# Optimization experiments

Hardware: AMD Instinct MI355X
Metric: run time of the kernel (lower is better)

Reference implementation:

```python
import jax, jax.numpy as jnp
import numpy as np

B, S, DIM = 2, 2048, 2048
H, DH = 16, 128            # head_dim = dim // n_heads; decop_rot_dim == head_dim (required by the view)
LKV, LQ = 512, 1024        # latent kv / q compression dims


def setup_inputs() -> dict:
    key = jax.random.key(0)
    ks = jax.random.split(key, 12)
    w = lambda k, shape: jax.random.normal(k, shape, jnp.float32) * 0.02
    x = jax.random.normal(ks[0], (B, S, DIM), jnp.float32)
    # rotary table: angles[t, i] = t * 10000^(-2i/DH), complex passed as cos/sin pair
    inv_freq = 1.0 / (10000.0 ** (np.arange(0, DH, 2, dtype=np.float64) / DH))
    ang = np.outer(np.arange(S, dtype=np.float64), inv_freq)  # [S, DH/2]
    return {
        "x": x,
        "freq_cos": jnp.asarray(np.cos(ang), jnp.float32),
        "freq_sin": jnp.asarray(np.sin(ang), jnp.float32),
        "w_lq": w(ks[1], (LQ, DIM)),
        "w_lkv": w(ks[2], (LKV, DIM)),
        "w_q": w(ks[3], (H * DH, LQ)),
        "w_k": w(ks[4], (H * DH, LKV)),
        "w_v": w(ks[5], (H * DH, LKV)),
        "w_qr": w(ks[6], (H * DH, LQ)),
        "b_qr": w(ks[7], (H * DH,)),
        "w_kr": w(ks[8], (H * DH, DIM)),
        "b_kr": w(ks[9], (H * DH,)),
        "w_o": w(ks[10], (DIM, H * DH)),
        "b_o": w(ks[11], (DIM,)),
    }


def _rope(t, freq):
    # t: [B,S,H,DH]; freq: [S,DH/2] complex. Pairs (even,odd) along last dim rotated.
    b, s, h, d = t.shape
    tc = t.astype(jnp.float32).reshape(b, s, h, d // 2, 2)
    tc = jax.lax.complex(tc[..., 0], tc[..., 1]) * freq[None, :, None, :]
    return jnp.stack([jnp.real(tc), jnp.imag(tc)], axis=-1).reshape(b, s, h, d).astype(t.dtype)


def reference(x, freq_cos, freq_sin, w_lq, w_lkv, w_q, w_k, w_v, w_qr, b_qr, w_kr, b_kr, w_o, b_o):
    b, s, _ = x.shape
    freq = jax.lax.complex(freq_cos, freq_sin)          # [S, DH/2]
    cq = x @ w_lq.T                                      # [B,S,LQ]
    ckv = x @ w_lkv.T                                    # [B,S,LKV]
    q = (cq @ w_q.T).reshape(b, s, H, DH)
    qr = _rope((cq @ w_qr.T + b_qr).reshape(b, s, H, DH), freq)
    k = (ckv @ w_k.T).reshape(b, s, H, DH)
    kr = _rope((x @ w_kr.T + b_kr).reshape(b, s, H, DH), freq)
    v = (ckv @ w_v.T).reshape(b, s, H, DH)
    q = jnp.concatenate([q, qr], axis=-1)                # [B,S,H,2*DH]
    k = jnp.concatenate([k, kr], axis=-1)
    # note: scale uses sqrt(head_dim), NOT sqrt(2*head_dim), faithful to source
    scores = jnp.einsum('bqhd,bkhd->bhqk', q, k) / jnp.sqrt(jnp.float32(DH))
    att = jax.nn.softmax(scores.astype(jnp.float32), axis=-1).astype(q.dtype)
    out = jnp.einsum('bhqk,bkhd->bqhd', att, v).reshape(b, s, H * DH)
    return out @ w_o.T + b_o
```

## Files before the change

kernel.cpp:

```cpp
#include <hip/hip_runtime.h>
#include <hip/hip_bf16.h>


#define Bb 2
#define Ss 2048
#define DIMd 2048
#define Hh 16
#define DHd 128

typedef __hip_bfloat16 bf16;
typedef __attribute__((ext_vector_type(8))) short short8;
typedef __attribute__((ext_vector_type(4))) float floatx4;

#define MFMA(a, b, c) __builtin_amdgcn_mfma_f32_16x16x32_bf16((a), (b), (c), 0, 0, 0)

__device__ __forceinline__ void async16(const bf16* g, bf16* l) {
  __builtin_amdgcn_global_load_lds(
      (const __attribute__((address_space(1))) unsigned int*)g,
      (__attribute__((address_space(3))) unsigned int*)l, 16, 0, 0);
}

__global__ __launch_bounds__(256) void cvt_all(
    const float* x, const float* wlq, const float* wlkv, const float* wq,
    const float* wqr, const float* wk, const float* wv, const float* wkr,
    const float* wo, bf16* dx, bf16* dwlq, bf16* dwlkv, bf16* dwq, bf16* dwqr,
    bf16* dwk, bf16* dwv, bf16* dwkr, bf16* dwo) {
  long i = (long)blockIdx.x * 256 + threadIdx.x;
  const float* src;
  bf16* dst;
  long base;
  if (i < 2097152L)      { src = x;    dst = dx;    base = 0; }
  else if (i < 2621440L) { src = wlq;  dst = dwlq;  base = 2097152L; }
  else if (i < 2883584L) { src = wlkv; dst = dwlkv; base = 2621440L; }
  else if (i < 3407872L) { src = wq;   dst = dwq;   base = 2883584L; }
  else if (i < 3932160L) { src = wqr;  dst = dwqr;  base = 3407872L; }
  else if (i < 4194304L) { src = wk;   dst = dwk;   base = 3932160L; }
  else if (i < 4456448L) { src = wv;   dst = dwv;   base = 4194304L; }
  else if (i < 5505024L) { src = wkr;  dst = dwkr;  base = 4456448L; }
  else                   { src = wo;   dst = dwo;   base = 5505024L; }
  long j = i - base;
  float4 f = ((const float4*)src)[j];
  union { ushort4 u4; bf16 h[4]; } cv;
  cv.h[0] = __float2bfloat16(f.x);
  cv.h[1] = __float2bfloat16(f.y);
  cv.h[2] = __float2bfloat16(f.z);
  cv.h[3] = __float2bfloat16(f.w);
  ((ushort4*)dst)[j] = cv.u4;
}

template <int MODE>
__device__ __forceinline__ void gemm_body(const bf16* __restrict__ A,
                                          const bf16* __restrict__ Bw,
                                          const float* __restrict__ bias,
                                          void* __restrict__ Cout,
                                          void* __restrict__ Cout2,
                                          const float* __restrict__ fco,
                                          const float* __restrict__ fsi,
                                          int M, int N, int K, int lda) {
  extern __shared__ __align__(16) bf16 smem[];
  bf16* As = smem;
  bf16* Bs = smem + 8192;
  const int tid = threadIdx.x;
  const int lane = tid & 63;
  const int w = tid >> 6;
  const int wm = w & 1, wn = w >> 1;
  const int m0 = blockIdx.y * 128, n0 = blockIdx.x * 128;
  const int lr = lane & 15, lg = lane >> 4;

  floatx4 acc[4][4];
#pragma unroll
  for (int mi = 0; mi < 4; ++mi)
#pragma unroll
    for (int ni = 0; ni < 4; ++ni)
#pragma unroll
      for (int r = 0; r < 4; ++r) acc[mi][ni][r] = 0.f;

  for (int k0 = 0; k0 < K; k0 += 64) {
    __syncthreads();
#pragma unroll
    for (int i = 0; i < 4; ++i) {
      int c = i * 256 + tid;
      int row = c >> 3;
      int cg = (c & 7) ^ (row & 7);
      async16(A + (size_t)(m0 + row) * lda + k0 + cg * 8, As + (i * 256 + w * 64) * 8);
      async16(Bw + (size_t)(n0 + row) * K + k0 + cg * 8, Bs + (i * 256 + w * 64) * 8);
    }
    __syncthreads();

#pragma unroll
    for (int ks = 0; ks < 2; ++ks) {
      short8 af[4], bfr[4];
#pragma unroll
      for (int mi = 0; mi < 4; ++mi) {
        int row = wm * 64 + mi * 16 + lr;
        af[mi] = *(const short8*)&As[row * 64 + (((ks * 4 + lg) ^ (lr & 7)) * 8)];
      }
#pragma unroll
      for (int ni = 0; ni < 4; ++ni) {
        int row = wn * 64 + ni * 16 + lr;
        bfr[ni] = *(const short8*)&Bs[row * 64 + (((ks * 4 + lg) ^ (lr & 7)) * 8)];
      }
#pragma unroll
      for (int mi = 0; mi < 4; ++mi)
#pragma unroll
        for (int ni = 0; ni < 4; ++ni)
          acc[mi][ni] = MFMA(af[mi], bfr[ni], acc[mi][ni]);
    }
  }

  if (MODE == 5 && n0 >= 2048) {
    __syncthreads();
#pragma unroll
    for (int mi = 0; mi < 4; ++mi)
#pragma unroll
      for (int ni = 0; ni < 4; ++ni)
#pragma unroll
        for (int r = 0; r < 4; ++r) {
          int ml = wm * 64 + mi * 16 + lg * 4 + r;
          int nl = wn * 64 + ni * 16 + lr;
          smem[ml * 129 + nl] = __float2bfloat16(acc[mi][ni][r]);
        }
    __syncthreads();
    int bb = m0 >> 11, s0 = m0 & 2047;
    int hh = (n0 - 2048) >> 7;
    short* vbase = (short*)Cout2 + ((size_t)(bb * Hh + hh) * 128) * Ss;
#pragma unroll
    for (int pa = 0; pa < 8; ++pa) {
      int d = pa * 16 + (tid >> 4);
      int sc = (tid & 15) * 8;
      short8 v;
#pragma unroll
      for (int i = 0; i < 8; ++i) v[i] = *(const short*)&smem[(sc + i) * 129 + d];
      *(short8*)(vbase + (size_t)d * Ss + s0 + sc) = v;
    }
    return;
  }

#pragma unroll
  for (int mi = 0; mi < 4; ++mi)
#pragma unroll
    for (int ni = 0; ni < 4; ++ni)
#pragma unroll
      for (int r = 0; r < 4; ++r) {
        int m = m0 + wm * 64 + mi * 16 + lg * 4 + r;
        int n = n0 + wn * 64 + ni * 16 + lr;
        float v = acc[mi][ni][r];
        int bb = m >> 11, s = m & 2047;
        if (MODE == 3) {
          v += bias[n];
          ((float*)Cout)[(size_t)m * N + n] = v;
        } else if (MODE == 4) {
          if (n < 2048) {
            int hh = n >> 7, d = n & 127;
            ((bf16*)Cout)[((size_t)((bb * Hh + hh) * Ss + s)) * 256 + d] =
                __float2bfloat16(v);
          } else {
            int n2 = n - 2048;
            int hh = n2 >> 7, d = n2 & 127;
            v += bias[n2];
            float vp = __shfl_xor(v, 1, 64);
            float co = fco[s * 64 + (d >> 1)];
            float sn = fsi[s * 64 + (d >> 1)];
            v = (d & 1) ? (v * co + vp * sn) : (v * co - vp * sn);
            ((bf16*)Cout)[((size_t)((bb * Hh + hh) * Ss + s)) * 256 + 128 + d] =
                __float2bfloat16(v);
          }
        } else if (MODE == 5) {
          int hh = n >> 7, d = n & 127;
          ((bf16*)Cout)[((size_t)((bb * Hh + hh) * Ss + s)) * 256 + d] =
              __float2bfloat16(v);
        } else if (MODE == 6) {
          if (n < 1536) {
            ((bf16*)Cout)[(size_t)m * 1536 + n] = __float2bfloat16(v);
          } else {
            int n2 = n - 1536;
            int hh = n2 >> 7, d = n2 & 127;
            v += bias[n2];
            float vp = __shfl_xor(v, 1, 64);
            float co = fco[s * 64 + (d >> 1)];
            float sn = fsi[s * 64 + (d >> 1)];
            v = (d & 1) ? (v * co + vp * sn) : (v * co - vp * sn);
            ((bf16*)Cout2)[((size_t)((bb * Hh + hh) * Ss + s)) * 256 + 128 + d] =
                __float2bfloat16(v);
          }
        }
      }
}

template <int MODE>
__global__ __launch_bounds__(256, 4) void gemm_bt(const bf16* __restrict__ A,
                                                  const bf16* __restrict__ Bw,
                                                  const float* __restrict__ bias,
                                                  void* __restrict__ Cout,
                                                  void* __restrict__ Cout2,
                                                  const float* __restrict__ fco,
                                                  const float* __restrict__ fsi,
                                                  int M, int N, int K, int lda) {
  gemm_body<MODE>(A, Bw, bias, Cout, Cout2, fco, fsi, M, N, K, lda);
}

__global__ __launch_bounds__(256, 4) void gemm_qkv(const bf16* __restrict__ ccat,
                                                   const bf16* __restrict__ wqcat,
                                                   const bf16* __restrict__ wkvcat,
                                                   const float* __restrict__ bqr,
                                                   void* __restrict__ qcat,
                                                   void* __restrict__ kcat,
                                                   void* __restrict__ vt,
                                                   const float* __restrict__ fco,
                                                   const float* __restrict__ fsi) {
  if (blockIdx.z == 0)
    gemm_body<4>(ccat, wqcat, bqr, qcat, nullptr, fco, fsi, 4096, 4096, 1024, 1536);
  else
    gemm_body<5>(ccat + 1024, wkvcat, nullptr, kcat, vt, nullptr, nullptr, 4096, 4096, 512, 1536);
}

__global__ __launch_bounds__(256) void flash_attn(const bf16* __restrict__ Q,
                                                  const bf16* __restrict__ Kc,
                                                  const bf16* __restrict__ Vt,
                                                  bf16* __restrict__ Oa) {
  const float SCALE = 0.08838834764831845f;
  __shared__ __align__(16) bf16 Ks[64 * 256];
  __shared__ __align__(16) bf16 Vs[128 * 64];
  __shared__ __align__(16) bf16 pbuf[4][16 * 64];

  const int lane = threadIdx.x & 63;
  const int w = threadIdx.x >> 6;
  const int lr = lane & 15, lg = lane >> 4;
  const int m7 = lr & 7;
  const int bh = blockIdx.x;
  const int b = bh >> 4, h = bh & 15;
  const int q0 = blockIdx.y * 64 + w * 16;

  const bf16* Qb = Q + (size_t)bh * Ss * 256;
  const bf16* Kb = Kc + (size_t)bh * Ss * 256;
  const bf16* Vb = Vt + (size_t)bh * 128 * Ss;

  short8 qf[8];
  {
    const short* Qrow = (const short*)Qb + (size_t)(q0 + lr) * 256;
#pragma unroll
    for (int kk = 0; kk < 8; ++kk) qf[kk] = *(const short8*)(Qrow + kk * 32 + lg * 8);
  }

  float l_r[4];
  floatx4 oacc[8];
#pragma unroll
  for (int r = 0; r < 4; ++r) l_r[r] = 0.f;
#pragma unroll
  for (int nb = 0; nb < 8; ++nb)
#pragma unroll
    for (int r = 0; r < 4; ++r) oacc[nb][r] = 0.f;

  for (int j0 = 0; j0 < Ss; j0 += 64) {
    __syncthreads();
#pragma unroll
    for (int i = 0; i < 8; ++i) {
      int r = w * 16 + i * 2 + (lane >> 5);
      int cg = (lane & 31) ^ (r & 7);
      async16(Kb + (size_t)(j0 + r) * 256 + cg * 8, Ks + (w * 16 + i * 2) * 256);
    }
#pragma unroll
    for (int i = 0; i < 4; ++i) {
      int r = w * 32 + i * 8 + (lane >> 3);
      int cg = (lane & 7) ^ (r & 7);
      async16(Vb + (size_t)r * Ss + j0 + cg * 8, Vs + (w * 32 + i * 8) * 64);
    }
    __syncthreads();

    floatx4 sf[4];
#pragma unroll
    for (int cb = 0; cb < 4; ++cb)
#pragma unroll
      for (int r = 0; r < 4; ++r) sf[cb][r] = 0.f;
#pragma unroll
    for (int cb = 0; cb < 4; ++cb) {
      const short* Krow = (const short*)Ks + (cb * 16 + lr) * 256;
#pragma unroll
      for (int kk = 0; kk < 8; ++kk) {
        short8 kf = *(const short8*)(Krow + ((4 * kk + lg) ^ m7) * 8);
        sf[cb] = MFMA(qf[kk], kf, sf[cb]);
      }
    }

#pragma unroll
    for (int r = 0; r < 4; ++r) {
      float p0 = __expf(sf[0][r] * SCALE);
      float p1 = __expf(sf[1][r] * SCALE);
      float p2 = __expf(sf[2][r] * SCALE);
      float p3 = __expf(sf[3][r] * SCALE);
      sf[0][r] = p0; sf[1][r] = p1; sf[2][r] = p2; sf[3][r] = p3;
      l_r[r] += (p0 + p1) + (p2 + p3);
    }

    bf16* pb = pbuf[w];
#pragma unroll
    for (int cb = 0; cb < 4; ++cb)
#pragma unroll
      for (int r = 0; r < 4; ++r) {
        int row = lg * 4 + r;
        int ch = (2 * cb + (lr >> 3)) ^ (row & 7);
        pb[row * 64 + ch * 8 + m7] = __float2bfloat16(sf[cb][r]);
      }
    short8 pa[2];
#pragma unroll
    for (int kb = 0; kb < 2; ++kb)
      pa[kb] = *(const short8*)((const short*)pb + lr * 64 + ((4 * kb + lg) ^ m7) * 8);

#pragma unroll
    for (int nb = 0; nb < 8; ++nb) {
#pragma unroll
      for (int kb = 0; kb < 2; ++kb) {
        short8 vf = *(const short8*)((const short*)Vs + (nb * 16 + lr) * 64 +
                                     ((4 * kb + lg) ^ m7) * 8);
        oacc[nb] = MFMA(pa[kb], vf, oacc[nb]);
      }
    }
  }

  float inv_l[4];
#pragma unroll
  for (int r = 0; r < 4; ++r) {
    float s = l_r[r];
    s += __shfl_xor(s, 1, 64);
    s += __shfl_xor(s, 2, 64);
    s += __shfl_xor(s, 4, 64);
    s += __shfl_xor(s, 8, 64);
    inv_l[r] = 1.f / s;
  }
#pragma unroll
  for (int nb = 0; nb < 8; ++nb)
#pragma unroll
    for (int r = 0; r < 4; ++r) {
      int s = q0 + lg * 4 + r;
      int d = nb * 16 + lr;
      Oa[((size_t)(b * Ss + s)) * (Hh * 128) + h * 128 + d] =
          __float2bfloat16(oacc[nb][r] * inv_l[r]);
    }
}

extern "C" void kernel_launch(void* const* d_in, const int* in_sizes, int n_in,
                              void* d_out, int out_size, void* d_ws, size_t ws_size,
                              hipStream_t stream) {
  const float* x    = (const float*)d_in[0];
  const float* fco  = (const float*)d_in[1];
  const float* fsi  = (const float*)d_in[2];
  const float* wlq  = (const float*)d_in[3];
  const float* wlkv = (const float*)d_in[4];
  const float* wq   = (const float*)d_in[5];
  const float* wk   = (const float*)d_in[6];
  const float* wv   = (const float*)d_in[7];
  const float* wqr  = (const float*)d_in[8];
  const float* bqr  = (const float*)d_in[9];
  const float* wkr  = (const float*)d_in[10];
  const float* bkr  = (const float*)d_in[11];
  const float* wo   = (const float*)d_in[12];
  const float* bo   = (const float*)d_in[13];

  char* ws = (char*)d_ws;
  size_t o = 0;
  bf16* x_b    = (bf16*)(ws + o); o += (size_t)Bb * Ss * DIMd * 2;
  bf16* wbig   = (bf16*)(ws + o); o += (size_t)3584 * 2048 * 2;
  bf16* wqcat  = (bf16*)(ws + o); o += (size_t)4096 * 1024 * 2;
  bf16* wkvcat = (bf16*)(ws + o); o += (size_t)4096 * 512 * 2;
  bf16* wo_b   = (bf16*)(ws + o); o += (size_t)2048 * 2048 * 2;
  bf16* ccat   = (bf16*)(ws + o); o += (size_t)4096 * 1536 * 2;
  bf16* qcat   = (bf16*)(ws + o); o += (size_t)Bb * Hh * Ss * 256 * 2;
  bf16* kcat   = (bf16*)(ws + o); o += (size_t)Bb * Hh * Ss * 256 * 2;
  bf16* vt     = (bf16*)(ws + o); o += (size_t)Bb * Hh * 128 * Ss * 2;
  bf16* attn   = (bf16*)(ws + o); o += (size_t)4096 * 2048 * 2;

  cvt_all<<<25600, 256, 0, stream>>>(
      x, wlq, wlkv, wq, wqr, wk, wv, wkr, wo,
      x_b,
      wbig,
      wbig + (size_t)1024 * 2048,
      wqcat,
      wqcat + (size_t)2048 * 1024,
      wkvcat,
      wkvcat + (size_t)2048 * 512,
      wbig + (size_t)1536 * 2048,
      wo_b);

  const int M = Bb * Ss;
  const int GEMM_LDS = 128 * 129 * 2;
  gemm_bt<6><<<dim3(28, 32), 256, GEMM_LDS, stream>>>(
      x_b, wbig, bkr, ccat, kcat, fco, fsi, M, 3584, 2048, 2048);
  gemm_qkv<<<dim3(32, 32, 2), 256, GEMM_LDS, stream>>>(
      ccat, wqcat, wkvcat, bqr, qcat, kcat, vt, fco, fsi);

  flash_attn<<<dim3(Bb * Hh, Ss / 64), 256, 0, stream>>>(qcat, kcat, vt, attn);

  gemm_bt<3><<<dim3(16, 32), 256, GEMM_LDS, stream>>>(
      attn, wo_b, bo, (float*)d_out, nullptr, nullptr, nullptr, M, 2048, 2048, 2048);
}
```

Baseline: 510.8 us.

## Rework flash attention around 32x32 MFMA with register-resident P via lane shuffles

The attention kernel now uses 32x32x16 bf16 MFMA with each wave handling 32 query rows, so a block covers 128 rows and the grid halves. S is computed transposed (K as the A operand), which lets P be packed to bf16 in registers and exchanged across half-waves with shuffles instead of a round trip through an LDS buffer. It also switches to exp2 with a folded scale and precomputes swizzled LDS pointers. The intent is to double K/V reuse per LDS load, cut instruction count and drop the P staging through LDS. In exchange it uses more registers (launch bounds set to 2 blocks) and launches fewer blocks, which lowers occupancy.

```diff
diff --git a/kernel.cpp b/kernel.cpp
--- a/kernel.cpp
+++ b/kernel.cpp
@@ -11,8 +11,10 @@
 typedef __hip_bfloat16 bf16;
 typedef __attribute__((ext_vector_type(8))) short short8;
 typedef __attribute__((ext_vector_type(4))) float floatx4;
+typedef __attribute__((ext_vector_type(16))) float floatx16;
 
 #define MFMA(a, b, c) __builtin_amdgcn_mfma_f32_16x16x32_bf16((a), (b), (c), 0, 0, 0)
+#define MFMA32(a, b, c) __builtin_amdgcn_mfma_f32_32x32x16_bf16((a), (b), (c), 0, 0, 0)
 
 __device__ __forceinline__ void async16(const bf16* g, bf16* l) {
   __builtin_amdgcn_global_load_lds(
@@ -214,42 +216,53 @@
     gemm_body<5>(ccat + 1024, wkvcat, nullptr, kcat, vt, nullptr, nullptr, 4096, 4096, 512, 1536);
 }
 
-__global__ __launch_bounds__(256) void flash_attn(const bf16* __restrict__ Q,
-                                                  const bf16* __restrict__ Kc,
-                                                  const bf16* __restrict__ Vt,
-                                                  bf16* __restrict__ Oa) {
-  const float SCALE = 0.08838834764831845f;
+__global__ __launch_bounds__(256, 2) void flash_attn(const bf16* __restrict__ Q,
+                                                     const bf16* __restrict__ Kc,
+                                                     const bf16* __restrict__ Vt,
+                                                     bf16* __restrict__ Oa) {
+  const float CE = 0.08838834764831845f * 1.4426950408889634f;
   __shared__ __align__(16) bf16 Ks[64 * 256];
   __shared__ __align__(16) bf16 Vs[128 * 64];
-  __shared__ __align__(16) bf16 pbuf[4][16 * 64];
 
   const int lane = threadIdx.x & 63;
   const int w = threadIdx.x >> 6;
-  const int lr = lane & 15, lg = lane >> 4;
-  const int m7 = lr & 7;
+  const int m = lane & 31;
+  const int hi = lane >> 5;
   const int bh = blockIdx.x;
   const int b = bh >> 4, h = bh & 15;
-  const int q0 = blockIdx.y * 64 + w * 16;
+  const int q0 = blockIdx.y * 128 + w * 32;
 
   const bf16* Qb = Q + (size_t)bh * Ss * 256;
   const bf16* Kb = Kc + (size_t)bh * Ss * 256;
   const bf16* Vb = Vt + (size_t)bh * 128 * Ss;
 
-  short8 qf[8];
+  short8 qf[16];
   {
-    const short* Qrow = (const short*)Qb + (size_t)(q0 + lr) * 256;
-#pragma unroll
-    for (int kk = 0; kk < 8; ++kk) qf[kk] = *(const short8*)(Qrow + kk * 32 + lg * 8);
+    const short* Qrow = (const short*)Qb + (size_t)(q0 + m) * 256 + hi * 8;
+#pragma unroll
+    for (int dt = 0; dt < 16; ++dt) qf[dt] = *(const short8*)(Qrow + dt * 16);
   }
 
-  float l_r[4];
-  floatx4 oacc[8];
-#pragma unroll
-  for (int r = 0; r < 4; ++r) l_r[r] = 0.f;
-#pragma unroll
-  for (int nb = 0; nb < 8; ++nb)
-#pragma unroll
-    for (int r = 0; r < 4; ++r) oacc[nb][r] = 0.f;
+  const int key = m & 7;
+  const short* kp[2][4];
+#pragma unroll
+  for (int cbt = 0; cbt < 2; ++cbt)
+#pragma unroll
+    for (int dl = 0; dl < 4; ++dl)
+      kp[cbt][dl] = (const short*)Ks + (cbt * 32 + m) * 256 + (((2 * dl + hi) ^ key) * 8);
+  const short* vp[4];
+#pragma unroll
+  for (int kb = 0; kb < 4; ++kb)
+    vp[kb] = (const short*)Vs + m * 64 + (((2 * kb + hi) ^ key) * 8);
+
+  float l = 0.f;
+  floatx16 oacc[4];
+#pragma unroll
+  for (int nb = 0; nb < 4; ++nb)
+#pragma unroll
+    for (int r = 0; r < 16; ++r) oacc[nb][r] = 0.f;
+
+  const bool lo = (lane < 32);
 
   for (int j0 = 0; j0 < Ss; j0 += 64) {
     __syncthreads();
@@ -267,75 +280,68 @@
     }
     __syncthreads();
 
-    floatx4 sf[4];
-#pragma unroll
-    for (int cb = 0; cb < 4; ++cb)
-#pragma unroll
-      for (int r = 0; r < 4; ++r) sf[cb][r] = 0.f;
-#pragma unroll
-    for (int cb = 0; cb < 4; ++cb) {
-      const short* Krow = (const short*)Ks + (cb * 16 + lr) * 256;
-#pragma unroll
-      for (int kk = 0; kk < 8; ++kk) {
-        short8 kf = *(const short8*)(Krow + ((4 * kk + lg) ^ m7) * 8);
-        sf[cb] = MFMA(qf[kk], kf, sf[cb]);
-      }
-    }
-
-#pragma unroll
-    for (int r = 0; r < 4; ++r) {
-      float p0 = __expf(sf[0][r] * SCALE);
-      float p1 = __expf(sf[1][r] * SCALE);
-      float p2 = __expf(sf[2][r] * SCALE);
-      float p3 = __expf(sf[3][r] * SCALE);
-      sf[0][r] = p0; sf[1][r] = p1; sf[2][r] = p2; sf[3][r] = p3;
-      l_r[r] += (p0 + p1) + (p2 + p3);
-    }
-
-    bf16* pb = pbuf[w];
-#pragma unroll
-    for (int cb = 0; cb < 4; ++cb)
-#pragma unroll
-      for (int r = 0; r < 4; ++r) {
-        int row = lg * 4 + r;
-        int ch = (2 * cb + (lr >> 3)) ^ (row & 7);
-        pb[row * 64 + ch * 8 + m7] = __float2bfloat16(sf[cb][r]);
-      }
-    short8 pa[2];
-#pragma unroll
-    for (int kb = 0; kb < 2; ++kb)
-      pa[kb] = *(const short8*)((const short*)pb + lr * 64 + ((4 * kb + lg) ^ m7) * 8);
-
-#pragma unroll
-    for (int nb = 0; nb < 8; ++nb) {
-#pragma unroll
-      for (int kb = 0; kb < 2; ++kb) {
-        short8 vf = *(const short8*)((const short*)Vs + (nb * 16 + lr) * 64 +
-                                     ((4 * kb + lg) ^ m7) * 8);
-        oacc[nb] = MFMA(pa[kb], vf, oacc[nb]);
+    floatx16 sf[2];
+#pragma unroll
+    for (int t = 0; t < 2; ++t)
+#pragma unroll
+      for (int r = 0; r < 16; ++r) sf[t][r] = 0.f;
+#pragma unroll
+    for (int cbt = 0; cbt < 2; ++cbt)
+#pragma unroll
+      for (int dt = 0; dt < 16; ++dt) {
+        short8 kf = *(const short8*)(kp[cbt][dt & 3] + (dt >> 2) * 64);
+        sf[cbt] = MFMA32(kf, qf[dt], sf[cbt]);
+      }
+
+    unsigned pk[2][8];
+#pragma unroll
+    for (int t = 0; t < 2; ++t)
+#pragma unroll
+      for (int rp = 0; rp < 8; ++rp) {
+        float p0 = exp2f(sf[t][2 * rp] * CE);
+        float p1 = exp2f(sf[t][2 * rp + 1] * CE);
+        l += p0 + p1;
+        bf16 b0 = __float2bfloat16(p0);
+        bf16 b1 = __float2bfloat16(p1);
+        pk[t][rp] = ((unsigned)*(const unsigned short*)&b1 << 16) |
+                    *(const unsigned short*)&b0;
+      }
+
+#pragma unroll
+    for (int kb = 0; kb < 4; ++kb) {
+      const int t = kb >> 1, b4 = (kb & 1) * 4;
+      unsigned x1 = lo ? pk[t][b4 + 2] : pk[t][b4];
+      unsigned y1 = (unsigned)__shfl_xor((int)x1, 32, 64);
+      unsigned x2 = lo ? pk[t][b4 + 3] : pk[t][b4 + 1];
+      unsigned y2 = (unsigned)__shfl_xor((int)x2, 32, 64);
+      union { unsigned u[4]; short8 s; } pa;
+      pa.u[0] = lo ? pk[t][b4] : y1;
+      pa.u[1] = lo ? pk[t][b4 + 1] : y2;
+      pa.u[2] = lo ? y1 : pk[t][b4 + 2];
+      pa.u[3] = lo ? y2 : pk[t][b4 + 3];
+#pragma unroll
+      for (int nb = 0; nb < 4; ++nb) {
+        short8 vf = *(const short8*)(vp[kb] + nb * 2048);
+        oacc[nb] = MFMA32(pa.s, vf, oacc[nb]);
       }
     }
   }
 
-  float inv_l[4];
-#pragma unroll
-  for (int r = 0; r < 4; ++r) {
-    float s = l_r[r];
-    s += __shfl_xor(s, 1, 64);
-    s += __shfl_xor(s, 2, 64);
-    s += __shfl_xor(s, 4, 64);
-    s += __shfl_xor(s, 8, 64);
-    inv_l[r] = 1.f / s;
+  float lsum = l + __shfl_xor(l, 32, 64);
+  float inv = 1.f / lsum;
+
+#pragma unroll
+  for (int r = 0; r < 16; ++r) {
+    int qr = (r & 3) + 8 * (r >> 2) + 4 * hi;
+    float invr = __shfl(inv, (lane & 32) + qr, 64);
+    int s = q0 + qr;
+#pragma unroll
+    for (int nb = 0; nb < 4; ++nb) {
+      int d = nb * 32 + m;
+      Oa[((size_t)(b * Ss + s)) * (Hh * 128) + h * 128 + d] =
+          __float2bfloat16(oacc[nb][r] * invr);
+    }
   }
-#pragma unroll
-  for (int nb = 0; nb < 8; ++nb)
-#pragma unroll
-    for (int r = 0; r < 4; ++r) {
-      int s = q0 + lg * 4 + r;
-      int d = nb * 16 + lr;
-      Oa[((size_t)(b * Ss + s)) * (Hh * 128) + h * 128 + d] =
-          __float2bfloat16(oacc[nb][r] * inv_l[r]);
-    }
 }
 
 extern "C" void kernel_launch(void* const* d_in, const int* in_sizes, int n_in,
@@ -388,7 +394,7 @@
   gemm_qkv<<<dim3(32, 32, 2), 256, GEMM_LDS, stream>>>(
       ccat, wqcat, wkvcat, bqr, qcat, kcat, vt, fco, fsi);
 
-  flash_attn<<<dim3(Bb * Hh, Ss / 64), 256, 0, stream>>>(qcat, kcat, vt, attn);
+  flash_attn<<<dim3(Bb * Hh, Ss / 128), 256, 0, stream>>>(qcat, kcat, vt, attn);
 
   gemm_bt<3><<<dim3(16, 32), 256, GEMM_LDS, stream>>>(
       attn, wo_b, bo, (float*)d_out, nullptr, nullptr, nullptr, M, 2048, 2048, 2048);
```

Result: faster. 459.4 us (-10.1%).
